# Kernel optimization log

Measured on AMD Instinct MI355X. Metric: run time of the kernel, lower is better.

Reference implementation:

```python
import jax, jax.numpy as jnp
import numpy as np

SINKHORN_ITERS = 50  # fixed iteration count (original uses err-tolerance while-loop)


def sinkhorn(M, a, b, lam):
    # M: [T, V] cost; a: [T, B] topic marginals; b: [V, B] word marginals
    K = jnp.exp(-M * lam)            # [T, V]
    u0 = jnp.ones_like(a) / a.shape[0]

    def step(u, _):
        v = b / (K.T @ u)            # [V, B]
        u = a / (K @ v)              # [T, B]
        return u, None

    u, _ = jax.lax.scan(step, u0, None, length=SINKHORN_ITERS)
    v = b / (K.T @ u)
    # per-document sinkhorn divergence: sum_t u_t * ((K*M) @ v)_t -> [B]
    return jnp.sum(u * ((K * M) @ v), axis=0)


def setup_inputs() -> dict:
    key = jax.random.key(0)
    kx, kt, kw, km, ke = jax.random.split(key, 5)
    B, T, V, E = 2048, 100, 20000, 256
    x = jax.random.uniform(kx, (B, V), dtype=jnp.float32)  # BoW-like weights
    doc_topic = jax.random.uniform(kt, (B, T), dtype=jnp.float32) + 1e-3
    doc_topic = doc_topic / jnp.sum(doc_topic, axis=1, keepdims=True)
    doc_word = jax.random.uniform(kw, (B, V), dtype=jnp.float32) + 1e-3
    doc_word = doc_word / jnp.sum(doc_word, axis=1, keepdims=True)
    M = jax.random.uniform(km, (T, V), dtype=jnp.float32)  # nonneg cost in [0,1)
    topic_embedding = jax.random.normal(ke, (T, E), dtype=jnp.float32)
    return {"x": x, "doc_topic": doc_topic, "doc_word": doc_word, "M": M,
            "topic_embedding": topic_embedding, "sh_alpha": 20,
            "rec_loss_weight": 100}


def reference(x, doc_topic, doc_word, M, topic_embedding, sh_alpha, rec_loss_weight):
    sh_loss = sinkhorn(M, doc_topic.T, doc_word.T, sh_alpha).mean()
    rec_log_probs = jax.nn.log_softmax(doc_topic @ (1.0 - M), axis=1)  # [B, V]
    rec_loss = -jnp.mean(jnp.sum(rec_log_probs * x, axis=1))
    joint_loss = rec_loss_weight * rec_loss + sh_loss
    return (rec_loss, sh_loss, joint_loss)
```

## Files before the change

### kernel.cpp

```cpp
#include <hip/hip_runtime.h>
#include <math.h>

#define B_   2048
#define T_   100
#define V_   20000
#define VP   20480
#define KP   128
#define TP   112
#define NC2  32
#define CH2  640
#define LDV  72
#define RXB  16

typedef short s8v __attribute__((ext_vector_type(8)));
typedef short s4v __attribute__((ext_vector_type(4)));
typedef float f4  __attribute__((ext_vector_type(4)));

__device__ __forceinline__ short f2bf(float f) {
    unsigned u = __builtin_bit_cast(unsigned, f);
    u += 0x7fffu + ((u >> 16) & 1u);
    return (short)(u >> 16);
}
__device__ __forceinline__ float bf2f(short h) {
    unsigned u = ((unsigned)(unsigned short)h) << 16;
    return __builtin_bit_cast(float, u);
}
#define MFMA(a,b,c) __builtin_amdgcn_mfma_f32_16x16x32_bf16((a),(b),(c),0,0,0)

__global__ void k_initKT(const float* __restrict__ M, const int* __restrict__ alpha,
                         short* __restrict__ A1, short* __restrict__ W1) {
    __shared__ float tile[32][33];
    float lam = (float)(*alpha);
    int v0 = blockIdx.x * 32, t0 = blockIdx.y * 32;
    int tx = threadIdx.x, ty = threadIdx.y;
    for (int j = 0; j < 4; ++j) {
        int t = t0 + ty + 8 * j, v = v0 + tx;
        tile[ty + 8 * j][tx] = (t < T_ && v < V_) ? M[(size_t)t * V_ + v] : 0.f;
    }
    __syncthreads();
    for (int j = 0; j < 4; ++j) {
        int t = t0 + tx, v = v0 + ty + 8 * j;
        float m = tile[tx][ty + 8 * j];
        bool valid = (t < T_) && (v < V_);
        A1[(size_t)v * KP + t] = valid ? f2bf(__expf(-m * lam)) : (short)0;
        W1[(size_t)v * KP + t] = valid ? f2bf(1.f - m) : (short)0;
    }
}

__global__ void k_initA2(const float* __restrict__ M, const int* __restrict__ alpha,
                         short* __restrict__ A2, short* __restrict__ A2M) {
    float lam = (float)(*alpha);
    size_t id = (size_t)blockIdx.x * 256 + threadIdx.x;
    int t = (int)(id / VP), v = (int)(id % VP);
    bool valid = (t < T_) && (v < V_);
    float m = valid ? M[(size_t)t * V_ + v] : 0.f;
    float k = valid ? __expf(-m * lam) : 0.f;
    A2[id]  = valid ? f2bf(k) : (short)0;
    A2M[id] = valid ? f2bf(k * m) : (short)0;
}

__global__ void k_init0(short* __restrict__ uTbf) {
    int id = blockIdx.x * 256 + threadIdx.x;
    int t = id & (KP - 1);
    uTbf[id] = (t < T_) ? f2bf(0.01f) : (short)0;
}

__global__ void k_castdw(const float* __restrict__ dw, short* __restrict__ dwbf) {
    size_t base = ((size_t)blockIdx.x * 256 + threadIdx.x) * 8;
    f4 x0 = __builtin_nontemporal_load((const f4*)(dw + base));
    f4 x1 = __builtin_nontemporal_load((const f4*)(dw + base + 4));
    s8v o;
    o[0]=f2bf(x0[0]); o[1]=f2bf(x0[1]); o[2]=f2bf(x0[2]); o[3]=f2bf(x0[3]);
    o[4]=f2bf(x1[0]); o[5]=f2bf(x1[1]); o[6]=f2bf(x1[2]); o[7]=f2bf(x1[3]);
    __builtin_nontemporal_store(o, (s8v*)(dwbf + base));
}

__global__ void k_castdt(const float* __restrict__ dt, short* __restrict__ dtbf) {
    int id = blockIdx.x * 256 + threadIdx.x;
    int b = id >> 7, t = id & (KP - 1);
    dtbf[id] = (t < T_) ? f2bf(dt[(size_t)b * T_ + t]) : (short)0;
}

__global__ __launch_bounds__(256, 2) void k_GF(const short* __restrict__ A1,
                                               const short* __restrict__ A2acc,
                                               const short* __restrict__ uT,
                                               const short* __restrict__ dwbf,
                                               float* __restrict__ part2) {
    __shared__ short vv[4][32 * LDV];
    int tid = threadIdx.x;
    int wave = tid >> 6, lane = tid & 63, q = lane >> 4, l16 = lane & 15;

    int l = blockIdx.x;
    int j = l & 31, bx = l >> 5;
    int c = ((j & 7) << 2) | (j >> 3);
    int v0 = c * CH2;
    int b0 = bx * 128 + wave * 32;
    short* buf = vv[wave];

    s8v au[2][4];
#pragma unroll
    for (int cb = 0; cb < 2; ++cb)
#pragma unroll
        for (int ks = 0; ks < 4; ++ks)
            au[cb][ks] = *(const s8v*)(uT + (size_t)(b0 + cb * 16 + l16) * KP + ks * 32 + q * 8);

    f4 acc2[7][2];
#pragma unroll
    for (int tt = 0; tt < 7; ++tt) { acc2[tt][0] = (f4)0.f; acc2[tt][1] = (f4)0.f; }

    for (int s = 0; s < 10; ++s) {
        int vs = v0 + s * 64;
        s4v dwv[2][4];
#pragma unroll
        for (int cb = 0; cb < 2; ++cb)
#pragma unroll
            for (int vt = 0; vt < 4; ++vt) {
                int vg = vs + vt * 16 + q * 4;
                dwv[cb][vt] = (vg < V_)
                    ? __builtin_nontemporal_load(
                          (const s4v*)(dwbf + (size_t)(b0 + cb * 16 + l16) * V_ + vg))
                    : (s4v)0;
            }
        s8v a2r[2][7];
#pragma unroll
        for (int ks2 = 0; ks2 < 2; ++ks2)
#pragma unroll
            for (int tt = 0; tt < 7; ++tt)
                a2r[ks2][tt] = *(const s8v*)(A2acc + (size_t)(tt * 16 + l16) * VP
                                             + vs + ks2 * 32 + q * 8);
        f4 acc1[2][4];
#pragma unroll
        for (int cb = 0; cb < 2; ++cb)
#pragma unroll
            for (int vt = 0; vt < 4; ++vt) acc1[cb][vt] = (f4)0.f;
#pragma unroll
        for (int ks = 0; ks < 4; ++ks) {
            int ko = ks * 32 + q * 8;
            s8v bv[4];
#pragma unroll
            for (int vt = 0; vt < 4; ++vt)
                bv[vt] = *(const s8v*)(A1 + (size_t)(vs + vt * 16 + l16) * KP + ko);
#pragma unroll
            for (int cb = 0; cb < 2; ++cb)
#pragma unroll
                for (int vt = 0; vt < 4; ++vt)
                    acc1[cb][vt] = MFMA(bv[vt], au[cb][ks], acc1[cb][vt]);
        }
#pragma unroll
        for (int cb = 0; cb < 2; ++cb)
#pragma unroll
            for (int vt = 0; vt < 4; ++vt) {
                int vg = vs + vt * 16 + q * 4;
                s4v o;
                if (vg < V_) {
#pragma unroll
                    for (int r = 0; r < 4; ++r)
                        o[r] = f2bf(bf2f(dwv[cb][vt][r]) * __builtin_amdgcn_rcpf(acc1[cb][vt][r]));
                } else {
                    o = (s4v)0;
                }
                *(s4v*)(buf + (cb * 16 + l16) * LDV + vt * 16 + q * 4) = o;
            }
#pragma unroll
        for (int ks2 = 0; ks2 < 2; ++ks2) {
            int ko = ks2 * 32 + q * 8;
            s8v bb[2];
#pragma unroll
            for (int cb = 0; cb < 2; ++cb)
                bb[cb] = *(const s8v*)(buf + (cb * 16 + l16) * LDV + ko);
#pragma unroll
            for (int tt = 0; tt < 7; ++tt)
#pragma unroll
                for (int cb = 0; cb < 2; ++cb)
                    acc2[tt][cb] = MFMA(a2r[ks2][tt], bb[cb], acc2[tt][cb]);
        }
        __builtin_amdgcn_s_barrier();
    }
#pragma unroll
    for (int tt = 0; tt < 7; ++tt)
#pragma unroll
        for (int cb = 0; cb < 2; ++cb) {
            int bg = b0 + cb * 16 + l16;
            __builtin_nontemporal_store(acc2[tt][cb],
                (f4*)(part2 + ((size_t)c * B_ + bg) * TP + tt * 16 + q * 4));
        }
}

__global__ void k_R(const float* __restrict__ part2, const float* __restrict__ dt,
                    float* __restrict__ uf, short* __restrict__ uTbf,
                    float* __restrict__ kmvf, int mode) {
    int id = blockIdx.x * 256 + threadIdx.x;
    int b = id / 28, t4 = (id % 28) * 4;
    f4 s = (f4)0.f;
    for (int c = 0; c < NC2; ++c)
        s += __builtin_nontemporal_load(
                 (const f4*)(part2 + ((size_t)c * B_ + b) * TP + t4));
    if (mode == 0) {
#pragma unroll
        for (int j = 0; j < 4; ++j) {
            int t = t4 + j;
            float v = (t < T_) ? dt[(size_t)b * T_ + t] / s[j] : 0.f;
            uf[(size_t)b * TP + t] = v;
            uTbf[(size_t)b * KP + t] = f2bf(v);
        }
    } else {
#pragma unroll
        for (int j = 0; j < 4; ++j) kmvf[(size_t)b * TP + t4 + j] = s[j];
    }
}

__global__ __launch_bounds__(256, 4) void k_rec(const short* __restrict__ dtbf,
                                                const short* __restrict__ W1,
                                                const float* __restrict__ x,
                                                float* __restrict__ recP) {
    int tid = threadIdx.x;
    int wave = tid >> 6, lane = tid & 63, q = lane >> 4, l16 = lane & 15;
    int xb = blockIdx.x;
    int v0 = xb * (RXB == 16 ? 1280 : 0);
    int b0 = blockIdx.y * 64;
    int bg = b0 + wave * 16 + l16;
    s8v a[4];
#pragma unroll
    for (int ks = 0; ks < 4; ++ks)
        a[ks] = *(const s8v*)(dtbf + (size_t)bg * KP + ks * 32 + q * 8);
    float se = 0.f, sxl = 0.f, sx = 0.f;
    for (int st = 0; st < 5; ++st) {
        int vs = v0 + st * 256;
        f4 acc[16];
#pragma unroll
        for (int vt = 0; vt < 16; ++vt) acc[vt] = (f4)0.f;
#pragma unroll
        for (int ks = 0; ks < 4; ++ks) {
            int ko = ks * 32 + q * 8;
#pragma unroll
            for (int vt = 0; vt < 16; ++vt) {
                s8v w = *(const s8v*)(W1 + (size_t)(vs + vt * 16 + l16) * KP + ko);
                acc[vt] = MFMA(w, a[ks], acc[vt]);
            }
        }
#pragma unroll
        for (int vt = 0; vt < 16; ++vt) {
            int vg = vs + vt * 16 + q * 4;
            if (vg < V_) {
                f4 xv = __builtin_nontemporal_load(
                            (const f4*)(x + (size_t)bg * V_ + vg));
#pragma unroll
                for (int r = 0; r < 4; ++r) {
                    float lo = acc[vt][r];
                    se += __expf(lo); sxl += lo * xv[r]; sx += xv[r];
                }
            }
        }
    }
    se  += __shfl_xor(se, 16, 64);  se  += __shfl_xor(se, 32, 64);
    sxl += __shfl_xor(sxl, 16, 64); sxl += __shfl_xor(sxl, 32, 64);
    sx  += __shfl_xor(sx, 16, 64);  sx  += __shfl_xor(sx, 32, 64);
    if (q == 0) {
        recP[((size_t)xb * 3 + 0) * B_ + bg] = se;
        recP[((size_t)xb * 3 + 1) * B_ + bg] = sxl;
        recP[((size_t)xb * 3 + 2) * B_ + bg] = sx;
    }
}

__global__ void k_div(const float* __restrict__ uf, const float* __restrict__ kmvf,
                      const float* __restrict__ recP, float* __restrict__ divb,
                      float* __restrict__ recSE, float* __restrict__ recSXL,
                      float* __restrict__ recSX) {
    int b = blockIdx.x * 256 + threadIdx.x;
    if (b >= B_) return;
    float s = 0.f;
    for (int t = 0; t < TP; ++t) s += uf[(size_t)b * TP + t] * kmvf[(size_t)b * TP + t];
    divb[b] = s;
    float se = 0.f, sxl = 0.f, sx = 0.f;
    for (int xb = 0; xb < RXB; ++xb) {
        se  += recP[((size_t)xb * 3 + 0) * B_ + b];
        sxl += recP[((size_t)xb * 3 + 1) * B_ + b];
        sx  += recP[((size_t)xb * 3 + 2) * B_ + b];
    }
    recSE[b] = se; recSXL[b] = sxl; recSX[b] = sx;
}

__global__ void k_final(const float* __restrict__ divb, const float* __restrict__ recSE,
                        const float* __restrict__ recSXL, const float* __restrict__ recSX,
                        const int* __restrict__ wptr, float* __restrict__ out) {
    __shared__ float sA[256], sB[256];
    int tid = threadIdx.x;
    float accS = 0.f, accR = 0.f;
    for (int b = tid; b < B_; b += 256) {
        accS += divb[b];
        accR += recSXL[b] - logf(recSE[b]) * recSX[b];
    }
    sA[tid] = accS; sB[tid] = accR;
    __syncthreads();
    for (int s = 128; s > 0; s >>= 1) {
        if (tid < s) { sA[tid] += sA[tid + s]; sB[tid] += sB[tid + s]; }
        __syncthreads();
    }
    if (tid == 0) {
        float sh = sA[0] / (float)B_;
        float rec = -sB[0] / (float)B_;
        out[0] = rec;
        out[1] = sh;
        out[2] = (float)(*wptr) * rec + sh;
    }
}

extern "C" void kernel_launch(void* const* d_in, const int* in_sizes, int n_in,
                              void* d_out, int out_size, void* d_ws, size_t ws_size,
                              hipStream_t stream) {
    const float* x  = (const float*)d_in[0];
    const float* dt = (const float*)d_in[1];
    const float* dw = (const float*)d_in[2];
    const float* M  = (const float*)d_in[3];
    const int* alpha = (const int*)d_in[5];
    const int* wrec  = (const int*)d_in[6];
    float* out = (float*)d_out;

    char* p = (char*)d_ws;
    short* A1   = (short*)p; p += (size_t)VP * KP * 2;
    short* W1   = (short*)p; p += (size_t)VP * KP * 2;
    short* A2   = (short*)p; p += (size_t)TP * VP * 2;
    short* A2M  = (short*)p; p += (size_t)TP * VP * 2;
    short* uTbf = (short*)p; p += (size_t)B_ * KP * 2;
    short* dtbf = (short*)p; p += (size_t)B_ * KP * 2;
    short* dwbf = (short*)p; p += (size_t)B_ * V_ * 2;
    float* part2 = (float*)p; p += (size_t)NC2 * B_ * TP * 4;
    float* uf    = (float*)p; p += (size_t)B_ * TP * 4;
    float* kmvf  = (float*)p; p += (size_t)B_ * TP * 4;
    float* recP  = (float*)p; p += (size_t)RXB * 3 * B_ * 4;
    float* recSE  = (float*)p; p += B_ * 4;
    float* recSXL = (float*)p; p += B_ * 4;
    float* recSX  = (float*)p; p += B_ * 4;
    float* divb   = (float*)p; p += B_ * 4;

    k_initKT<<<dim3(VP / 32, 4), dim3(32, 8), 0, stream>>>(M, alpha, A1, W1);
    k_initA2<<<(TP * VP) / 256, 256, 0, stream>>>(M, alpha, A2, A2M);
    k_init0<<<(B_ * KP) / 256, 256, 0, stream>>>(uTbf);
    k_castdw<<<(B_ * V_) / (256 * 8), 256, 0, stream>>>(dw, dwbf);
    k_castdt<<<(B_ * KP) / 256, 256, 0, stream>>>(dt, dtbf);
    k_rec<<<dim3(RXB, B_ / 64), 256, 0, stream>>>(dtbf, W1, x, recP);

    for (int it = 0; it < 50; ++it) {
        k_GF<<<dim3((B_ / 128) * NC2), 256, 0, stream>>>(A1, A2, uTbf, dwbf, part2);
        k_R<<<(B_ * 28) / 256, 256, 0, stream>>>(part2, dt, uf, uTbf, kmvf, 0);
    }
    k_GF<<<dim3((B_ / 128) * NC2), 256, 0, stream>>>(A1, A2M, uTbf, dwbf, part2);
    k_R<<<(B_ * 28) / 256, 256, 0, stream>>>(part2, dt, uf, uTbf, kmvf, 1);
    k_div<<<B_ / 256, 256, 0, stream>>>(uf, kmvf, recP, divb, recSE, recSXL, recSX);
    k_final<<<1, 256, 0, stream>>>(divb, recSE, recSXL, recSX, wrec, out);
}
```

Before: 5.677 ms.

## Prefetch doc-word tiles in sinkhorn kernel and split rec kernel into finer blocks

In the sinkhorn V-side kernel, the next 64-column slice of doc_word is loaded into registers one iteration ahead, so global load latency overlaps the MFMA work. The per-iteration barrier is removed and the loads become regular cached loads instead of nontemporal ones. The reconstruction kernel now has each block handle a single 256-word slice with 79 blocks along V, and its x tile is loaded before the MFMA loop. This gives more blocks and earlier memory traffic, at the cost of more register pressure (launch bounds lowered to 2) and more partial-result rows for the reduction to combine.

```diff
diff --git a/kernel.cpp b/kernel.cpp
--- a/kernel.cpp
+++ b/kernel.cpp
@@ -10,7 +10,7 @@
 #define NC2  32
 #define CH2  640
 #define LDV  72
-#define RXB  16
+#define RXB  79
 
 typedef short s8v __attribute__((ext_vector_type(8)));
 typedef short s4v __attribute__((ext_vector_type(4)));
@@ -108,19 +108,32 @@
 #pragma unroll
     for (int tt = 0; tt < 7; ++tt) { acc2[tt][0] = (f4)0.f; acc2[tt][1] = (f4)0.f; }
 
+    s4v dwv[2][4];
+#pragma unroll
+    for (int cb = 0; cb < 2; ++cb)
+#pragma unroll
+        for (int vt = 0; vt < 4; ++vt) {
+            int vg = v0 + vt * 16 + q * 4;
+            dwv[cb][vt] = (vg < V_)
+                ? *(const s4v*)(dwbf + (size_t)(b0 + cb * 16 + l16) * V_ + vg)
+                : (s4v)0;
+        }
+
     for (int s = 0; s < 10; ++s) {
         int vs = v0 + s * 64;
-        s4v dwv[2][4];
-#pragma unroll
-        for (int cb = 0; cb < 2; ++cb)
-#pragma unroll
-            for (int vt = 0; vt < 4; ++vt) {
-                int vg = vs + vt * 16 + q * 4;
-                dwv[cb][vt] = (vg < V_)
-                    ? __builtin_nontemporal_load(
-                          (const s4v*)(dwbf + (size_t)(b0 + cb * 16 + l16) * V_ + vg))
-                    : (s4v)0;
-            }
+        s4v dwn[2][4];
+        if (s < 9) {
+            int vn = vs + 64;
+#pragma unroll
+            for (int cb = 0; cb < 2; ++cb)
+#pragma unroll
+                for (int vt = 0; vt < 4; ++vt) {
+                    int vg = vn + vt * 16 + q * 4;
+                    dwn[cb][vt] = (vg < V_)
+                        ? *(const s4v*)(dwbf + (size_t)(b0 + cb * 16 + l16) * V_ + vg)
+                        : (s4v)0;
+                }
+        }
         s8v a2r[2][7];
 #pragma unroll
         for (int ks2 = 0; ks2 < 2; ++ks2)
@@ -174,7 +187,10 @@
                 for (int cb = 0; cb < 2; ++cb)
                     acc2[tt][cb] = MFMA(a2r[ks2][tt], bb[cb], acc2[tt][cb]);
         }
-        __builtin_amdgcn_s_barrier();
+#pragma unroll
+        for (int cb = 0; cb < 2; ++cb)
+#pragma unroll
+            for (int vt = 0; vt < 4; ++vt) dwv[cb][vt] = dwn[cb][vt];
     }
 #pragma unroll
     for (int tt = 0; tt < 7; ++tt)
@@ -209,46 +225,47 @@
     }
 }
 
-__global__ __launch_bounds__(256, 4) void k_rec(const short* __restrict__ dtbf,
+__global__ __launch_bounds__(256, 2) void k_rec(const short* __restrict__ dtbf,
                                                 const short* __restrict__ W1,
                                                 const float* __restrict__ x,
                                                 float* __restrict__ recP) {
     int tid = threadIdx.x;
     int wave = tid >> 6, lane = tid & 63, q = lane >> 4, l16 = lane & 15;
     int xb = blockIdx.x;
-    int v0 = xb * (RXB == 16 ? 1280 : 0);
+    int v0 = xb * 256;
     int b0 = blockIdx.y * 64;
     int bg = b0 + wave * 16 + l16;
+    f4 xv[16];
+#pragma unroll
+    for (int vt = 0; vt < 16; ++vt) {
+        int vg = v0 + vt * 16 + q * 4;
+        xv[vt] = (vg < V_) ? *(const f4*)(x + (size_t)bg * V_ + vg) : (f4)0.f;
+    }
     s8v a[4];
 #pragma unroll
     for (int ks = 0; ks < 4; ++ks)
         a[ks] = *(const s8v*)(dtbf + (size_t)bg * KP + ks * 32 + q * 8);
+    f4 acc[16];
+#pragma unroll
+    for (int vt = 0; vt < 16; ++vt) acc[vt] = (f4)0.f;
+#pragma unroll
+    for (int ks = 0; ks < 4; ++ks) {
+        int ko = ks * 32 + q * 8;
+#pragma unroll
+        for (int vt = 0; vt < 16; ++vt) {
+            s8v w = *(const s8v*)(W1 + (size_t)(v0 + vt * 16 + l16) * KP + ko);
+            acc[vt] = MFMA(w, a[ks], acc[vt]);
+        }
+    }
     float se = 0.f, sxl = 0.f, sx = 0.f;
-    for (int st = 0; st < 5; ++st) {
-        int vs = v0 + st * 256;
-        f4 acc[16];
-#pragma unroll
-        for (int vt = 0; vt < 16; ++vt) acc[vt] = (f4)0.f;
-#pragma unroll
-        for (int ks = 0; ks < 4; ++ks) {
-            int ko = ks * 32 + q * 8;
-#pragma unroll
-            for (int vt = 0; vt < 16; ++vt) {
-                s8v w = *(const s8v*)(W1 + (size_t)(vs + vt * 16 + l16) * KP + ko);
-                acc[vt] = MFMA(w, a[ks], acc[vt]);
-            }
-        }
-#pragma unroll
-        for (int vt = 0; vt < 16; ++vt) {
-            int vg = vs + vt * 16 + q * 4;
-            if (vg < V_) {
-                f4 xv = __builtin_nontemporal_load(
-                            (const f4*)(x + (size_t)bg * V_ + vg));
-#pragma unroll
-                for (int r = 0; r < 4; ++r) {
-                    float lo = acc[vt][r];
-                    se += __expf(lo); sxl += lo * xv[r]; sx += xv[r];
-                }
+#pragma unroll
+    for (int vt = 0; vt < 16; ++vt) {
+        int vg = v0 + vt * 16 + q * 4;
+        if (vg < V_) {
+#pragma unroll
+            for (int r = 0; r < 4; ++r) {
+                float lo = acc[vt][r];
+                se += __expf(lo); sxl += lo * xv[vt][r]; sx += xv[vt][r];
             }
         }
     }
```

After: 5.061 ms. -10.8%, faster.
